# Performance work log

Hardware: AMD Instinct MI355X
Metric: run time of the kernel (lower is better)

## Reference

```python
import jax, jax.numpy as jnp
import numpy as np

N = 100000   # nodes
E = 1600000  # edges per view
F = 256      # feature_dim
G = 512      # num graphs in batch
H, C = 2, 32 # heads, channels per head (GATConv(F, 32, heads=2))
EPS = 1e-5


def setup_inputs() -> dict:
    key = jax.random.key(0)
    ks = jax.random.split(key, 32)
    def w(i, shape, fan_in):
        return jax.random.normal(ks[i], shape, jnp.float32) / np.sqrt(fan_in)
    inp = {
        "x": jax.random.normal(ks[0], (N, F), jnp.float32),
        "edge_index_ast": jax.random.randint(ks[1], (2, E), 0, N),
        "edge_index_cfg": jax.random.randint(ks[2], (2, E), 0, N),
        "edge_index_pdg": jax.random.randint(ks[3], (2, E), 0, N),
        "batch": jnp.sort(jax.random.randint(ks[4], (N,), 0, G)),
        "num_graphs": G,
        # BatchNorm1d(feature_dim) affine params (training-mode batch stats)
        "bn_w": jnp.ones((F,), jnp.float32),
        "bn_b": jnp.zeros((F,), jnp.float32),
    }
    i = 5
    for v in ("ast", "cfg", "pdg"):
        inp[f"{v}_W"] = w(i, (F, H * C), F); i += 1
        inp[f"{v}_att_src"] = w(i, (H, C), C); i += 1
        inp[f"{v}_att_dst"] = w(i, (H, C), C); i += 1
        inp[f"{v}_bias"] = jnp.zeros((H * C,), jnp.float32)
    inp["g1_w"] = w(i, (64, 32), 64); i += 1
    inp["g1_b"] = jnp.zeros((32,), jnp.float32)
    inp["g2_w"] = w(i, (32, 3), 32); i += 1
    inp["g2_b"] = jnp.zeros((3,), jnp.float32)
    inp["c1_w"] = w(i, (64, 128), 64); i += 1
    inp["c1_b"] = jnp.zeros((128,), jnp.float32)
    inp["c2_w"] = w(i, (128, 64), 128); i += 1
    inp["c2_b"] = jnp.zeros((64,), jnp.float32)
    inp["c3_w"] = w(i, (64, 1), 64); i += 1
    inp["c3_b"] = jnp.zeros((1,), jnp.float32)
    return inp


def _gat(x, edge_index, W, att_src, att_dst, bias):
    """PyG GATConv (shared lin, add_self_loops=True, concat heads)."""
    n = x.shape[0]
    loops = jnp.arange(n)
    src = jnp.concatenate([edge_index[0], loops])
    dst = jnp.concatenate([edge_index[1], loops])
    h = (x @ W).reshape(n, H, C)                       # [N,H,C]
    a_src = jnp.sum(h * att_src, axis=-1)              # [N,H]
    a_dst = jnp.sum(h * att_dst, axis=-1)              # [N,H]
    e = jax.nn.leaky_relu(a_src[src] + a_dst[dst], 0.2)  # [Etot,H]
    m = jax.ops.segment_max(e, dst, num_segments=n)
    p = jnp.exp(e - m[dst])
    denom = jax.ops.segment_sum(p, dst, num_segments=n)
    alpha = p / (denom[dst] + 1e-16)                   # [Etot,H]
    out = jax.ops.segment_sum(h[src] * alpha[:, :, None], dst, num_segments=n)
    return out.reshape(n, H * C) + bias


def reference(x, edge_index_ast, edge_index_cfg, edge_index_pdg, batch, num_graphs,
              bn_w, bn_b,
              ast_W, ast_att_src, ast_att_dst, ast_bias,
              cfg_W, cfg_att_src, cfg_att_dst, cfg_bias,
              pdg_W, pdg_att_src, pdg_att_dst, pdg_bias,
              g1_w, g1_b, g2_w, g2_b,
              c1_w, c1_b, c2_w, c2_b, c3_w, c3_b):
    # input BatchNorm1d (training-mode batch statistics, biased variance)
    mu = x.mean(0)
    var = x.var(0)
    xn = (x - mu) / jnp.sqrt(var + EPS) * bn_w + bn_b

    h_ast = jax.ops.segment_max(jax.nn.elu(_gat(xn, edge_index_ast, ast_W, ast_att_src, ast_att_dst, ast_bias)), batch, num_segments=num_graphs)
    h_cfg = jax.ops.segment_max(jax.nn.elu(_gat(xn, edge_index_cfg, cfg_W, cfg_att_src, cfg_att_dst, cfg_bias)), batch, num_segments=num_graphs)
    h_pdg = jax.ops.segment_max(jax.nn.elu(_gat(xn, edge_index_pdg, pdg_W, pdg_att_src, pdg_att_dst, pdg_bias)), batch, num_segments=num_graphs)

    avg_view = (h_ast + h_cfg + h_pdg) / 3.0
    wts = jax.nn.softmax(jax.nn.relu(avg_view @ g1_w + g1_b) @ g2_w + g2_b, axis=-1)
    fused = wts[:, 0:1] * h_ast + wts[:, 1:2] * h_cfg + wts[:, 2:3] * h_pdg

    # classifier (dropout = identity at inference)
    z = jax.nn.relu(fused @ c1_w + c1_b)
    z = jax.nn.relu(z @ c2_w + c2_b)
    logits = (z @ c3_w + c3_b).reshape(-1)             # [G]
    return logits
```

## Files before the change

### kernel.cpp

```cpp
#include <hip/hip_runtime.h>
#include <hip/hip_bf16.h>
#include <hip/hip_fp16.h>

#define N_NODES 100000
#define N_EDGES 1600000
#define ETOT    (N_EDGES + N_NODES)
#define NE3     (3 * ETOT)
#define N3      (3 * N_NODES)
#define NF      256
#define NG      512
#define NHC     64
#define NOUT3   192
#define BN_EPS  1e-5f

#define NBUCK   586
#define NB1     1024
#define EGRAIN  20
#define ECHUNK  (256 * EGRAIN)
#define SCAN_N  (NBUCK * NB1)
#define ATT_NB  (N3 * 16 / 256)

typedef _Float16 f16x8 __attribute__((ext_vector_type(8)));
typedef float    f32x4 __attribute__((ext_vector_type(4)));

__device__ __forceinline__ unsigned fenc(float f){
  unsigned b = __float_as_uint(f);
  return (b & 0x80000000u) ? ~b : (b | 0x80000000u);
}
__device__ __forceinline__ float fdec(unsigned u){
  unsigned b = (u & 0x80000000u) ? (u & 0x7FFFFFFFu) : ~u;
  return __uint_as_float(b);
}
__device__ __forceinline__ float lrelu(float x){ return x > 0.f ? x : 0.2f * x; }
__device__ __forceinline__ float eluf(float x){ return x > 0.f ? x : (__expf(x) - 1.f); }

__global__ void k_init_pooled(unsigned* pooled){
  int i = blockIdx.x * 256 + threadIdx.x;
  if (i < 3 * NG * NHC) pooled[i] = 0x007FFFFFu;
}

#define STATS_NB ((N_NODES + 127) / 128)
__global__ __launch_bounds__(256) void k_pre(const float* __restrict__ x,
                                             float* __restrict__ sums, float* __restrict__ sumsq,
                                             const int* __restrict__ eA, const int* __restrict__ eC,
                                             const int* __restrict__ eP,
                                             int* __restrict__ gcounts){
  int t = threadIdx.x;
  if (blockIdx.x < STATS_NB){
    int r0 = blockIdx.x * 128;
    int rmax = N_NODES - r0; if (rmax > 128) rmax = 128;
    float s = 0.f, q = 0.f;
    for (int r = 0; r < rmax; ++r){
      float v = x[(size_t)(r0 + r) * NF + t];
      s += v; q += v * v;
    }
    atomicAdd(&sums[t], s);
    atomicAdd(&sumsq[t], q);
    return;
  }
  __shared__ int hist[NBUCK];
  int bi = blockIdx.x - STATS_NB;
  for (int b = t; b < NBUCK; b += 256) hist[b] = 0;
  __syncthreads();
  int base = bi * ECHUNK + t;
#pragma unroll
  for (int k = 0; k < EGRAIN; ++k){
    int i = base + k * 256;
    if (i < NE3){
      int v = i / ETOT; int j = i - v * ETOT;
      const int* ei = (v == 0) ? eA : (v == 1) ? eC : eP;
      int d = (j < N_EDGES) ? ei[N_EDGES + j] : (j - N_EDGES);
      int vd = v * N_NODES + d;
      atomicAdd(&hist[vd >> 9], 1);
    }
  }
  __syncthreads();
  for (int b = t; b < NBUCK; b += 256) gcounts[b * NB1 + bi] = hist[b];
}

__global__ __launch_bounds__(256) void k_prep2(const float* __restrict__ sums, const float* __restrict__ sumsq,
                                               const float* __restrict__ bn_w, const float* __restrict__ bn_b,
                                               const float* __restrict__ WA, const float* __restrict__ WC,
                                               const float* __restrict__ WP,
                                               __half* __restrict__ WpT, float* __restrict__ bp){
  __shared__ float red[256];
  int o = blockIdx.x;
  int v = o >> 6, oc = o & 63;
  const float* W = (v == 0) ? WA : (v == 1) ? WC : WP;
  int f = threadIdx.x;
  float mu  = sums[f]  * (1.f / N_NODES);
  float var = sumsq[f] * (1.f / N_NODES) - mu * mu;
  float sc  = bn_w[f] * rsqrtf(var + BN_EPS);
  float sh_ = bn_b[f] - mu * sc;
  float w = W[f * 64 + oc];
  WpT[(size_t)o * NF + f] = __float2half(w * sc);
  red[f] = sh_ * w;
  __syncthreads();
  for (int off = 128; off > 0; off >>= 1){
    if (f < off) red[f] += red[f + off];
    __syncthreads();
  }
  if (f == 0) bp[o] = red[0];
}

__global__ __launch_bounds__(256) void k_scan1(const int* __restrict__ cnt, int* __restrict__ out,
                                               int* __restrict__ bsum, int n){
  __shared__ int sh[256];
  int t = threadIdx.x; int base = blockIdx.x * 2048 + t * 8;
  int v[8]; int s = 0;
#pragma unroll
  for (int i = 0; i < 8; ++i){ v[i] = (base + i < n) ? cnt[base + i] : 0; s += v[i]; }
  sh[t] = s; __syncthreads();
  for (int off = 1; off < 256; off <<= 1){
    int xv = (t >= off) ? sh[t - off] : 0;
    __syncthreads();
    sh[t] += xv;
    __syncthreads();
  }
  int p = sh[t] - s;
  if (t == 255) bsum[blockIdx.x] = sh[255];
#pragma unroll
  for (int i = 0; i < 8; ++i){ if (base + i < n) out[base + i] = p; p += v[i]; }
}

__global__ __launch_bounds__(512) void k_scan2(int* __restrict__ bsum, int* __restrict__ total_out, int nb){
  __shared__ int sh[512];
  int t = threadIdx.x;
  int o = (t < nb) ? bsum[t] : 0;
  sh[t] = o; __syncthreads();
  for (int off = 1; off < 512; off <<= 1){
    int xv = (t >= off) ? sh[t - off] : 0;
    __syncthreads();
    sh[t] += xv;
    __syncthreads();
  }
  if (t < nb) bsum[t] = sh[t] - o;
  if (t == nb - 1) total_out[0] = sh[t];
}

__global__ __launch_bounds__(256) void k_scan3(int* __restrict__ out, const int* __restrict__ bsum, int n){
  int add = bsum[blockIdx.x];
  int base = blockIdx.x * 2048 + threadIdx.x * 8;
#pragma unroll
  for (int i = 0; i < 8; ++i) if (base + i < n) out[base + i] += add;
}

#define GBM 64
#define GEMM_NB ((N_NODES + GBM - 1) / GBM)
__global__ __launch_bounds__(256) void k_fused(const float* __restrict__ x,
                                               const __half* __restrict__ WpT, const float* __restrict__ bp,
                                               __half* __restrict__ h16,
                                               const int* __restrict__ eA, const int* __restrict__ eC,
                                               const int* __restrict__ eP,
                                               const int* __restrict__ gscan, int* __restrict__ packed){
  union U { _Float16 xs[64 * 256]; int pos[NBUCK]; };
  __shared__ U sm;
  int t = threadIdx.x;
  if (blockIdx.x >= GEMM_NB){
    int bi = blockIdx.x - GEMM_NB;
    for (int b = t; b < NBUCK; b += 256) sm.pos[b] = gscan[b * NB1 + bi];
    __syncthreads();
    int base = bi * ECHUNK + t;
#pragma unroll
    for (int k = 0; k < EGRAIN; ++k){
      int i = base + k * 256;
      if (i < NE3){
        int v = i / ETOT; int j = i - v * ETOT;
        const int* ei = (v == 0) ? eA : (v == 1) ? eC : eP;
        int s, d;
        if (j < N_EDGES){ s = ei[j]; d = ei[N_EDGES + j]; } else { s = j - N_EDGES; d = s; }
        int vd = v * N_NODES + d;
        int p = atomicAdd(&sm.pos[vd >> 9], 1);
        packed[p] = s | ((vd & 511) << 17);
      }
    }
    return;
  }
  int m0 = blockIdx.x * GBM;
#pragma unroll
  for (int k = 0; k < 8; ++k){
    int G = t + k * 256;
    int row = G >> 5, g = G & 31;
    int grow = m0 + row; if (grow >= N_NODES) grow = N_NODES - 1;
    const float4* src = (const float4*)(x + (size_t)grow * NF + ((g ^ (row & 7)) << 3));
    float4 lo = src[0], hi = src[1];
    f16x8 h;
    h[0]=(_Float16)lo.x; h[1]=(_Float16)lo.y; h[2]=(_Float16)lo.z; h[3]=(_Float16)lo.w;
    h[4]=(_Float16)hi.x; h[5]=(_Float16)hi.y; h[6]=(_Float16)hi.z; h[7]=(_Float16)hi.w;
    *(f16x8*)&sm.xs[(size_t)G << 3] = h;
  }
  __syncthreads();
  int lane = t & 63, w = t >> 6;
  int lr = lane & 15, lk = lane >> 4;
  int colb = w * 48;
  f32x4 acc[4][3];
#pragma unroll
  for (int mt = 0; mt < 4; ++mt)
#pragma unroll
    for (int ct = 0; ct < 3; ++ct) acc[mt][ct] = (f32x4){0.f, 0.f, 0.f, 0.f};
  float bpv[3];
#pragma unroll
  for (int ct = 0; ct < 3; ++ct) bpv[ct] = bp[colb + ct * 16 + lr];
#pragma unroll
  for (int kk = 0; kk < 8; ++kk){
    int khalf = kk * 32 + lk * 8;
    f16x8 av[4];
#pragma unroll
    for (int mt = 0; mt < 4; ++mt){
      int row = mt * 16 + lr;
      av[mt] = *(const f16x8*)&sm.xs[row * 256 + (khalf ^ ((row & 7) << 3))];
    }
    f16x8 bv[3];
#pragma unroll
    for (int ct = 0; ct < 3; ++ct){
      int col = colb + ct * 16 + lr;
      bv[ct] = *(const f16x8*)(const void*)(WpT + (size_t)col * NF + khalf);
    }
#pragma unroll
    for (int mt = 0; mt < 4; ++mt)
#pragma unroll
      for (int ct = 0; ct < 3; ++ct)
        acc[mt][ct] = __builtin_amdgcn_mfma_f32_16x16x32_f16(av[mt], bv[ct], acc[mt][ct], 0, 0, 0);
  }
#pragma unroll
  for (int mt = 0; mt < 4; ++mt){
#pragma unroll
    for (int r = 0; r < 4; ++r){
      int row = m0 + mt * 16 + lk * 4 + r;
      if (row < N_NODES){
#pragma unroll
        for (int ct = 0; ct < 3; ++ct)
          h16[(size_t)row * NOUT3 + colb + ct * 16 + lr] = __float2half(acc[mt][ct][r] + bpv[ct]);
      }
    }
  }
}

__global__ __launch_bounds__(256) void k_build(const int* __restrict__ gscan, const int* __restrict__ packed,
                                               int* __restrict__ entries, int* __restrict__ offsets){
  __shared__ int hist2[512];
  __shared__ int sh[256];
  int b = blockIdx.x, t = threadIdx.x;
  int base = gscan[b * NB1];
  int end  = (b == NBUCK - 1) ? NE3 : gscan[(b + 1) * NB1];
  hist2[t * 2] = 0; hist2[t * 2 + 1] = 0;
  __syncthreads();
  for (int i = base + t; i < end; i += 256)
    atomicAdd(&hist2[(packed[i] >> 17) & 511], 1);
  __syncthreads();
  int s0 = hist2[t * 2], s1 = hist2[t * 2 + 1];
  int tot = s0 + s1;
  sh[t] = tot; __syncthreads();
  for (int off = 1; off < 256; off <<= 1){
    int xv = (t >= off) ? sh[t - off] : 0;
    __syncthreads();
    sh[t] += xv;
    __syncthreads();
  }
  int p = sh[t] - tot;
  hist2[t * 2]     = p;
  hist2[t * 2 + 1] = p + s0;
  __syncthreads();
#pragma unroll
  for (int i = 0; i < 2; ++i){
    int vd = (b << 9) + t * 2 + i;
    if (vd < N3) offsets[vd] = base + hist2[t * 2 + i];
  }
  if (b == NBUCK - 1 && t == 0) offsets[N3] = NE3;
  __syncthreads();
  for (int i = base + t; i < end; i += 256){
    int pk = packed[i];
    int low = (pk >> 17) & 511;
    int pos = atomicAdd(&hist2[low], 1);
    entries[base + pos] = pk & 0x1FFFF;
  }
}

__global__ __launch_bounds__(256) void k_att(const __half* __restrict__ h16,
                                             const float* __restrict__ asA, const float* __restrict__ adA,
                                             const float* __restrict__ asC, const float* __restrict__ adC,
                                             const float* __restrict__ asP, const float* __restrict__ adP,
                                             float* __restrict__ a_src, float* __restrict__ a_dst,
                                             unsigned* __restrict__ gpart){
  __shared__ unsigned samax[6];
  int t = threadIdx.x;
  if (t < 6) samax[t] = 0u;
  __syncthreads();
  int gt = blockIdx.x * 256 + t;
  int g = gt >> 4; int lid = gt & 15;
  int v = g / N_NODES; int n = g - v * N_NODES;
  const float* As = (v == 0) ? asA : (v == 1) ? asC : asP;
  const float* Ad = (v == 0) ? adA : (v == 1) ? adC : adP;
  const __half2* hp = (const __half2*)(h16 + (size_t)n * NOUT3 + v * 64 + lid * 4);
  float2 fa = __half22float2(hp[0]);
  float2 fb = __half22float2(hp[1]);
  float4 s4 = *(const float4*)(As + lid * 4);
  float4 d4 = *(const float4*)(Ad + lid * 4);
  float rs = fa.x*s4.x + fa.y*s4.y + fb.x*s4.z + fb.y*s4.w;
  float rd = fa.x*d4.x + fa.y*d4.y + fb.x*d4.z + fb.y*d4.w;
  rs += __shfl_xor(rs, 1); rd += __shfl_xor(rd, 1);
  rs += __shfl_xor(rs, 2); rd += __shfl_xor(rd, 2);
  rs += __shfl_xor(rs, 4); rd += __shfl_xor(rd, 4);
  if ((lid & 7) == 0){
    int h = lid >> 3;
    a_src[g * 2 + h] = rs;
    a_dst[g * 2 + h] = rd;
    atomicMax(&samax[v * 2 + h], fenc(rs));
  }
  __syncthreads();
  if (t < 6) gpart[blockIdx.x * 6 + t] = samax[t];
}

__global__ __launch_bounds__(256) void k_amax(const unsigned* __restrict__ gpart, unsigned* __restrict__ amax){
  __shared__ unsigned sm[6];
  int t = threadIdx.x;
  if (t < 6) sm[t] = 0u;
  __syncthreads();
  unsigned m[6] = {0u, 0u, 0u, 0u, 0u, 0u};
  for (int bi = t; bi < ATT_NB; bi += 256){
    const unsigned* p = gpart + (size_t)bi * 6;
#pragma unroll
    for (int k = 0; k < 6; ++k) m[k] = max(m[k], p[k]);
  }
#pragma unroll
  for (int k = 0; k < 6; ++k) atomicMax(&sm[k], m[k]);
  __syncthreads();
  if (t < 6) amax[t] = sm[t];
}

__global__ __launch_bounds__(256) void k_gather(const int* __restrict__ entries, const int* __restrict__ offsets,
                                                const float* __restrict__ a_src, const float* __restrict__ a_dst,
                                                const unsigned* __restrict__ amax,
                                                const __half* __restrict__ h16,
                                                const float* __restrict__ bA, const float* __restrict__ bC,
                                                const float* __restrict__ bP,
                                                const int* __restrict__ batch, unsigned* __restrict__ pooled){
  __shared__ unsigned red[64];
  __shared__ int kmin, kmax;
  int t = threadIdx.x;
  if (t == 0){ kmin = 0x7FFFFFFF; kmax = -1; }
  if (t < 64) red[t] = 0u;
  __syncthreads();
  int grp = t >> 4;
  int lid = t & 15;
  int g = blockIdx.x * 16 + grp;
  int v = g / N_NODES; int n = g - v * N_NODES;
  int vN = v * N_NODES;
  float ad0 = a_dst[g*2+0], ad1 = a_dst[g*2+1];
  float m0 = lrelu(fdec(amax[v*2+0]) + ad0);
  float m1 = lrelu(fdec(amax[v*2+1]) + ad1);
  int beg = offsets[g], end = offsets[g+1];
  int len = end - beg;
  float ax = 0.f, ay = 0.f, az = 0.f, aw = 0.f;
  float den0 = 0.f, den1 = 0.f;
  const __half* hbase = h16 + v * 64 + lid * 4;
  for (int c0 = 0; c0 < len; c0 += 16){
    int nc = len - c0; if (nc > 16) nc = 16;
    int s_ = 0; float p0 = 0.f, p1 = 0.f;
    if (lid < nc){
      s_ = entries[beg + c0 + lid];
      float2 ap = *(const float2*)(a_src + (size_t)(vN + s_) * 2);
      p0 = __expf(lrelu(ap.x + ad0) - m0);
      p1 = __expf(lrelu(ap.y + ad1) - m1);
    }
    den0 += p0; den1 += p1;
    for (int k = 0; k < nc; k += 4){
      uint2 r[4]; float pav[4], pbv[4];
#pragma unroll
      for (int j = 0; j < 4; ++j){
        int kk = k + j;
        int sk = __shfl(s_, kk, 16);
        r[j] = *(const uint2*)(hbase + (size_t)sk * NOUT3);
        pav[j] = __shfl(p0, kk, 16);
        pbv[j] = __shfl(p1, kk, 16);
      }
#pragma unroll
      for (int j = 0; j < 4; ++j){
        int kk = k + j;
        if (kk < nc){
          float ph = (lid < 8) ? pav[j] : pbv[j];
          float2 fa2 = __half22float2(*(__half2*)&r[j].x);
          float2 fb2 = __half22float2(*(__half2*)&r[j].y);
          ax += ph * fa2.x; ay += ph * fa2.y; az += ph * fb2.x; aw += ph * fb2.y;
        }
      }
    }
  }
#pragma unroll
  for (int msk = 1; msk < 16; msk <<= 1){
    den0 += __shfl_xor(den0, msk);
    den1 += __shfl_xor(den1, msk);
  }
  float den = ((lid < 8) ? den0 : den1) + 1e-16f;
  const float* bias = (v == 0) ? bA : (v == 1) ? bC : bP;
  float4 b4 = *(const float4*)(bias + lid * 4);
  unsigned e0u = fenc(eluf(ax / den + b4.x));
  unsigned e1u = fenc(eluf(ay / den + b4.y));
  unsigned e2u = fenc(eluf(az / den + b4.z));
  unsigned e3u = fenc(eluf(aw / den + b4.w));
  int key = v * NG + batch[n];
  if (lid == 0){ atomicMin(&kmin, key); atomicMax(&kmax, key); }
  atomicMax(&red[lid*4+0], e0u); atomicMax(&red[lid*4+1], e1u);
  atomicMax(&red[lid*4+2], e2u); atomicMax(&red[lid*4+3], e3u);
  __syncthreads();
  if (kmin == kmax){
    if (t < 64) atomicMax(&pooled[(size_t)kmin * 64 + t], red[t]);
  } else {
    unsigned* pp = pooled + (size_t)key * 64 + lid * 4;
    atomicMax(pp+0, e0u); atomicMax(pp+1, e1u); atomicMax(pp+2, e2u); atomicMax(pp+3, e3u);
  }
}

__global__ __launch_bounds__(64) void k_head(const unsigned* __restrict__ pooled,
                                             const float* __restrict__ g1w, const float* __restrict__ g1b,
                                             const float* __restrict__ g2w, const float* __restrict__ g2b,
                                             const float* __restrict__ c1w, const float* __restrict__ c1b,
                                             const float* __restrict__ c2w, const float* __restrict__ c2b,
                                             const float* __restrict__ c3w, const float* __restrict__ c3b,
                                             float* __restrict__ out){
  __shared__ float s1[64];
  __shared__ float s2[128];
  __shared__ float sw[3];
  int g = blockIdx.x, l = threadIdx.x;
  float ha = fdec(pooled[(size_t)g * 64 + l]);
  float hc = fdec(pooled[(size_t)(NG + g) * 64 + l]);
  float hp = fdec(pooled[(size_t)(2 * NG + g) * 64 + l]);
  s1[l] = (ha + hc + hp) * (1.f / 3.f);
  __syncthreads();
  float r1 = 0.f;
  if (l < 32){
    r1 = g1b[l];
    for (int i = 0; i < 64; ++i) r1 += s1[i] * g1w[i * 32 + l];
    r1 = fmaxf(r1, 0.f);
  }
  __syncthreads();
  if (l < 32) s2[l] = r1;
  __syncthreads();
  if (l < 3){
    float tv = g2b[l];
    for (int i = 0; i < 32; ++i) tv += s2[i] * g2w[i * 3 + l];
    sw[l] = tv;
  }
  __syncthreads();
  float t0 = sw[0], t1 = sw[1], t2 = sw[2];
  float mx = fmaxf(t0, fmaxf(t1, t2));
  float w0 = __expf(t0 - mx), w1 = __expf(t1 - mx), w2 = __expf(t2 - mx);
  float wsum = w0 + w1 + w2;
  float fused = (w0 * ha + w1 * hc + w2 * hp) / wsum;
  __syncthreads();
  s1[l] = fused;
  __syncthreads();
  float za = c1b[l], zb = c1b[64 + l];
  for (int i = 0; i < 64; ++i){
    float f = s1[i];
    za += f * c1w[i * 128 + l];
    zb += f * c1w[i * 128 + 64 + l];
  }
  za = fmaxf(za, 0.f); zb = fmaxf(zb, 0.f);
  s2[l] = za; s2[64 + l] = zb;
  __syncthreads();
  float z2 = c2b[l];
  for (int i = 0; i < 128; ++i) z2 += s2[i] * c2w[i * 64 + l];
  z2 = fmaxf(z2, 0.f);
  float prod = z2 * c3w[l];
  for (int off = 32; off > 0; off >>= 1) prod += __shfl_down(prod, off);
  if (l == 0) out[g] = prod + c3b[0];
}

extern "C" void kernel_launch(void* const* d_in, const int* in_sizes, int n_in,
                              void* d_out, int out_size, void* d_ws, size_t ws_size,
                              hipStream_t stream){
  const float* x    = (const float*)d_in[0];
  const int* eA     = (const int*)d_in[1];
  const int* eC     = (const int*)d_in[2];
  const int* eP     = (const int*)d_in[3];
  const int* batch  = (const int*)d_in[4];
  const float* bn_w = (const float*)d_in[6];
  const float* bn_b = (const float*)d_in[7];
  const float* WA   = (const float*)d_in[8];
  const float* asA  = (const float*)d_in[9];
  const float* adA  = (const float*)d_in[10];
  const float* bA   = (const float*)d_in[11];
  const float* WC   = (const float*)d_in[12];
  const float* asC  = (const float*)d_in[13];
  const float* adC  = (const float*)d_in[14];
  const float* bC   = (const float*)d_in[15];
  const float* WP   = (const float*)d_in[16];
  const float* asP  = (const float*)d_in[17];
  const float* adP  = (const float*)d_in[18];
  const float* bP   = (const float*)d_in[19];
  const float* g1w  = (const float*)d_in[20];
  const float* g1b  = (const float*)d_in[21];
  const float* g2w  = (const float*)d_in[22];
  const float* g2b  = (const float*)d_in[23];
  const float* c1w  = (const float*)d_in[24];
  const float* c1b  = (const float*)d_in[25];
  const float* c2w  = (const float*)d_in[26];
  const float* c2b  = (const float*)d_in[27];
  const float* c3w  = (const float*)d_in[28];
  const float* c3b  = (const float*)d_in[29];
  float* out = (float*)d_out;

  char* wptr = (char*)d_ws;
  auto alloc = [&](size_t bytes) -> void* {
    void* p = (void*)wptr;
    wptr += (bytes + 255) & ~(size_t)255;
    return p;
  };
  float*    sums    = (float*)   alloc((size_t)NF * 4);
  float*    sumsq   = (float*)   alloc((size_t)NF * 4);
  size_t zbytes = (size_t)(wptr - (char*)sums);
  int*      gcounts = (int*)     alloc((size_t)SCAN_N * 4);
  int*      gscan   = (int*)     alloc((size_t)SCAN_N * 4);
  int*      offsets = (int*)     alloc(((size_t)N3 + 1) * 4);
  __half*   WpT     = (__half*)  alloc((size_t)NOUT3 * NF * 2);
  float*    bp      = (float*)   alloc((size_t)NOUT3 * 4);
  __half*   h16     = (__half*)  alloc((size_t)N_NODES * NOUT3 * 2);
  float*    a_src   = (float*)   alloc((size_t)N3 * 2 * 4);
  float*    a_dst   = (float*)   alloc((size_t)N3 * 2 * 4);
  int*      packed  = (int*)     alloc((size_t)NE3 * 4);
  int*      entries = (int*)     alloc((size_t)NE3 * 4);
  unsigned* pooled  = (unsigned*)alloc((size_t)3 * NG * NHC * 4);
  unsigned* gpart   = (unsigned*)alloc((size_t)ATT_NB * 6 * 4);
  unsigned* amax    = (unsigned*)alloc((size_t)64 * 4);
  int*      bsum    = (int*)     alloc((size_t)512 * 4);
  int*      scrtot  = (int*)     alloc((size_t)64 * 4);

  hipMemsetAsync(sums, 0, zbytes, stream);
  k_init_pooled<<<(3 * NG * NHC + 255) / 256, 256, 0, stream>>>(pooled);
  k_pre<<<STATS_NB + NB1, 256, 0, stream>>>(x, sums, sumsq, eA, eC, eP, gcounts);
  k_prep2<<<NOUT3, 256, 0, stream>>>(sums, sumsq, bn_w, bn_b, WA, WC, WP, WpT, bp);
  int nb_sc = (SCAN_N + 2047) / 2048;
  k_scan1<<<nb_sc, 256, 0, stream>>>(gcounts, gscan, bsum, SCAN_N);
  k_scan2<<<1, 512, 0, stream>>>(bsum, scrtot, nb_sc);
  k_scan3<<<nb_sc, 256, 0, stream>>>(gscan, bsum, SCAN_N);
  k_fused<<<GEMM_NB + NB1, 256, 0, stream>>>(x, WpT, bp, h16, eA, eC, eP, gscan, packed);
  k_att<<<ATT_NB, 256, 0, stream>>>(h16, asA, adA, asC, adC, asP, adP, a_src, a_dst, gpart);
  k_amax<<<1, 256, 0, stream>>>(gpart, amax);
  k_build<<<NBUCK, 256, 0, stream>>>(gscan, packed, entries, offsets);
  k_gather<<<N3 / 16, 256, 0, stream>>>(entries, offsets, a_src, a_dst, amax, h16, bA, bC, bP, batch, pooled);
  k_head<<<NG, 64, 0, stream>>>(pooled, g1w, g1b, g2w, g2b, c1w, c1b, c2w, c2b, c3w, c3b, out);
}
```

Before: 377.5 us.

## Widen CSR buckets, fuse amax into build, deterministic BN stats, unroll gather

Several independent changes ship together. Buckets now cover 1024 destination nodes each, halving the bucket count, and k_build runs 512 threads per block; the separate single-block k_amax reduction is folded into block 0 of k_build. BatchNorm column sums are written as per-block partials and reduced by a new k_stats2 kernel, which replaces global atomics and the memset. The gather inner loop is unrolled by 8 using precomputed byte offsets and FMAs, and drops the per-element bound check: out-of-range lanes carry zero weight and load row 0, so some loads are wasted.

```diff
diff --git a/kernel.cpp b/kernel.cpp
--- a/kernel.cpp
+++ b/kernel.cpp
@@ -13,7 +13,7 @@
 #define NOUT3   192
 #define BN_EPS  1e-5f
 
-#define NBUCK   586
+#define NBUCK   293
 #define NB1     1024
 #define EGRAIN  20
 #define ECHUNK  (256 * EGRAIN)
@@ -41,7 +41,7 @@
 
 #define STATS_NB ((N_NODES + 127) / 128)
 __global__ __launch_bounds__(256) void k_pre(const float* __restrict__ x,
-                                             float* __restrict__ sums, float* __restrict__ sumsq,
+                                             float* __restrict__ spartS, float* __restrict__ spartQ,
                                              const int* __restrict__ eA, const int* __restrict__ eC,
                                              const int* __restrict__ eP,
                                              int* __restrict__ gcounts){
@@ -54,8 +54,8 @@
       float v = x[(size_t)(r0 + r) * NF + t];
       s += v; q += v * v;
     }
-    atomicAdd(&sums[t], s);
-    atomicAdd(&sumsq[t], q);
+    spartS[(size_t)t * STATS_NB + blockIdx.x] = s;
+    spartQ[(size_t)t * STATS_NB + blockIdx.x] = q;
     return;
   }
   __shared__ int hist[NBUCK];
@@ -71,11 +71,29 @@
       const int* ei = (v == 0) ? eA : (v == 1) ? eC : eP;
       int d = (j < N_EDGES) ? ei[N_EDGES + j] : (j - N_EDGES);
       int vd = v * N_NODES + d;
-      atomicAdd(&hist[vd >> 9], 1);
+      atomicAdd(&hist[vd >> 10], 1);
     }
   }
   __syncthreads();
   for (int b = t; b < NBUCK; b += 256) gcounts[b * NB1 + bi] = hist[b];
+}
+
+__global__ __launch_bounds__(256) void k_stats2(const float* __restrict__ spartS, const float* __restrict__ spartQ,
+                                                float* __restrict__ sums, float* __restrict__ sumsq){
+  __shared__ float rs[256], rq[256];
+  int c = blockIdx.x, i = threadIdx.x;
+  float s = 0.f, q = 0.f;
+  for (int b = i; b < STATS_NB; b += 256){
+    s += spartS[(size_t)c * STATS_NB + b];
+    q += spartQ[(size_t)c * STATS_NB + b];
+  }
+  rs[i] = s; rq[i] = q;
+  __syncthreads();
+  for (int off = 128; off > 0; off >>= 1){
+    if (i < off){ rs[i] += rs[i + off]; rq[i] += rq[i + off]; }
+    __syncthreads();
+  }
+  if (i == 0){ sums[c] = rs[0]; sumsq[c] = rq[0]; }
 }
 
 __global__ __launch_bounds__(256) void k_prep2(const float* __restrict__ sums, const float* __restrict__ sumsq,
@@ -170,8 +188,8 @@
         int s, d;
         if (j < N_EDGES){ s = ei[j]; d = ei[N_EDGES + j]; } else { s = j - N_EDGES; d = s; }
         int vd = v * N_NODES + d;
-        int p = atomicAdd(&sm.pos[vd >> 9], 1);
-        packed[p] = s | ((vd & 511) << 17);
+        int p = atomicAdd(&sm.pos[vd >> 10], 1);
+        packed[p] = s | ((vd & 1023) << 17);
       }
     }
     return;
@@ -233,46 +251,6 @@
           h16[(size_t)row * NOUT3 + colb + ct * 16 + lr] = __float2half(acc[mt][ct][r] + bpv[ct]);
       }
     }
-  }
-}
-
-__global__ __launch_bounds__(256) void k_build(const int* __restrict__ gscan, const int* __restrict__ packed,
-                                               int* __restrict__ entries, int* __restrict__ offsets){
-  __shared__ int hist2[512];
-  __shared__ int sh[256];
-  int b = blockIdx.x, t = threadIdx.x;
-  int base = gscan[b * NB1];
-  int end  = (b == NBUCK - 1) ? NE3 : gscan[(b + 1) * NB1];
-  hist2[t * 2] = 0; hist2[t * 2 + 1] = 0;
-  __syncthreads();
-  for (int i = base + t; i < end; i += 256)
-    atomicAdd(&hist2[(packed[i] >> 17) & 511], 1);
-  __syncthreads();
-  int s0 = hist2[t * 2], s1 = hist2[t * 2 + 1];
-  int tot = s0 + s1;
-  sh[t] = tot; __syncthreads();
-  for (int off = 1; off < 256; off <<= 1){
-    int xv = (t >= off) ? sh[t - off] : 0;
-    __syncthreads();
-    sh[t] += xv;
-    __syncthreads();
-  }
-  int p = sh[t] - tot;
-  hist2[t * 2]     = p;
-  hist2[t * 2 + 1] = p + s0;
-  __syncthreads();
-#pragma unroll
-  for (int i = 0; i < 2; ++i){
-    int vd = (b << 9) + t * 2 + i;
-    if (vd < N3) offsets[vd] = base + hist2[t * 2 + i];
-  }
-  if (b == NBUCK - 1 && t == 0) offsets[N3] = NE3;
-  __syncthreads();
-  for (int i = base + t; i < end; i += 256){
-    int pk = packed[i];
-    int low = (pk >> 17) & 511;
-    int pos = atomicAdd(&hist2[low], 1);
-    entries[base + pos] = pk & 0x1FFFF;
   }
 }
 
@@ -311,21 +289,57 @@
   if (t < 6) gpart[blockIdx.x * 6 + t] = samax[t];
 }
 
-__global__ __launch_bounds__(256) void k_amax(const unsigned* __restrict__ gpart, unsigned* __restrict__ amax){
-  __shared__ unsigned sm[6];
-  int t = threadIdx.x;
-  if (t < 6) sm[t] = 0u;
-  __syncthreads();
-  unsigned m[6] = {0u, 0u, 0u, 0u, 0u, 0u};
-  for (int bi = t; bi < ATT_NB; bi += 256){
-    const unsigned* p = gpart + (size_t)bi * 6;
-#pragma unroll
-    for (int k = 0; k < 6; ++k) m[k] = max(m[k], p[k]);
-  }
-#pragma unroll
-  for (int k = 0; k < 6; ++k) atomicMax(&sm[k], m[k]);
-  __syncthreads();
-  if (t < 6) amax[t] = sm[t];
+__global__ __launch_bounds__(512) void k_build(const int* __restrict__ gscan, const int* __restrict__ packed,
+                                               int* __restrict__ entries, int* __restrict__ offsets,
+                                               const unsigned* __restrict__ gpart, unsigned* __restrict__ amax){
+  __shared__ int hist2[1024];
+  __shared__ int sh[512];
+  __shared__ unsigned smx[6];
+  int b = blockIdx.x, t = threadIdx.x;
+  if (b == 0){
+    if (t < 6) smx[t] = 0u;
+    __syncthreads();
+    unsigned m[6] = {0u, 0u, 0u, 0u, 0u, 0u};
+    for (int bi = t; bi < ATT_NB; bi += 512){
+      const unsigned* p = gpart + (size_t)bi * 6;
+#pragma unroll
+      for (int k = 0; k < 6; ++k) m[k] = max(m[k], p[k]);
+    }
+#pragma unroll
+    for (int k = 0; k < 6; ++k) atomicMax(&smx[k], m[k]);
+    __syncthreads();
+    if (t < 6) amax[t] = smx[t];
+  }
+  int base = gscan[b * NB1];
+  int end  = (b == NBUCK - 1) ? NE3 : gscan[(b + 1) * NB1];
+  hist2[t * 2] = 0; hist2[t * 2 + 1] = 0;
+  __syncthreads();
+  for (int i = base + t; i < end; i += 512)
+    atomicAdd(&hist2[(packed[i] >> 17) & 1023], 1);
+  __syncthreads();
+  int s0 = hist2[t * 2], s1 = hist2[t * 2 + 1];
+  int tot = s0 + s1;
+  sh[t] = tot; __syncthreads();
+  for (int off = 1; off < 512; off <<= 1){
+    int xv = (t >= off) ? sh[t - off] : 0;
+    __syncthreads();
+    sh[t] += xv;
+    __syncthreads();
+  }
+  int excl = sh[t] - tot;
+  hist2[t * 2]     = excl;
+  hist2[t * 2 + 1] = excl + s0;
+  int vd0 = (b << 10) + t * 2;
+  if (vd0 < N3)     offsets[vd0]     = base + excl;
+  if (vd0 + 1 < N3) offsets[vd0 + 1] = base + excl + s0;
+  if (b == NBUCK - 1 && t == 0) offsets[N3] = NE3;
+  __syncthreads();
+  for (int i = base + t; i < end; i += 512){
+    int pk = packed[i];
+    int low = (pk >> 17) & 1023;
+    int pos = atomicAdd(&hist2[low], 1);
+    entries[base + pos] = pk & 0x1FFFF;
+  }
 }
 
 __global__ __launch_bounds__(256) void k_gather(const int* __restrict__ entries, const int* __restrict__ offsets,
@@ -353,36 +367,37 @@
   int len = end - beg;
   float ax = 0.f, ay = 0.f, az = 0.f, aw = 0.f;
   float den0 = 0.f, den1 = 0.f;
-  const __half* hbase = h16 + v * 64 + lid * 4;
+  const char* hb = (const char*)h16;
+  unsigned lconst = (unsigned)((v << 7) + (lid << 3));
   for (int c0 = 0; c0 < len; c0 += 16){
     int nc = len - c0; if (nc > 16) nc = 16;
-    int s_ = 0; float p0 = 0.f, p1 = 0.f;
+    unsigned off_ = 0u;
+    float p0f = 0.f, p1f = 0.f;
     if (lid < nc){
-      s_ = entries[beg + c0 + lid];
+      int s_ = entries[beg + c0 + lid];
       float2 ap = *(const float2*)(a_src + (size_t)(vN + s_) * 2);
-      p0 = __expf(lrelu(ap.x + ad0) - m0);
-      p1 = __expf(lrelu(ap.y + ad1) - m1);
-    }
-    den0 += p0; den1 += p1;
-    for (int k = 0; k < nc; k += 4){
-      uint2 r[4]; float pav[4], pbv[4];
-#pragma unroll
-      for (int j = 0; j < 4; ++j){
+      p0f = __expf(lrelu(ap.x + ad0) - m0);
+      p1f = __expf(lrelu(ap.y + ad1) - m1);
+      off_ = (unsigned)s_ * (NOUT3 * 2);
+    }
+    den0 += p0f; den1 += p1f;
+    for (int k = 0; k < nc; k += 8){
+      uint2 r[8]; float pa[8];
+#pragma unroll
+      for (int j = 0; j < 8; ++j){
         int kk = k + j;
-        int sk = __shfl(s_, kk, 16);
-        r[j] = *(const uint2*)(hbase + (size_t)sk * NOUT3);
-        pav[j] = __shfl(p0, kk, 16);
-        pbv[j] = __shfl(p1, kk, 16);
+        unsigned ob = (unsigned)__shfl((int)off_, kk, 16) + lconst;
+        float pA = __shfl(p0f, kk, 16);
+        float pB = __shfl(p1f, kk, 16);
+        r[j] = *(const uint2*)(hb + ob);
+        pa[j] = (lid < 8) ? pA : pB;
       }
 #pragma unroll
-      for (int j = 0; j < 4; ++j){
-        int kk = k + j;
-        if (kk < nc){
-          float ph = (lid < 8) ? pav[j] : pbv[j];
-          float2 fa2 = __half22float2(*(__half2*)&r[j].x);
-          float2 fb2 = __half22float2(*(__half2*)&r[j].y);
-          ax += ph * fa2.x; ay += ph * fa2.y; az += ph * fb2.x; aw += ph * fb2.y;
-        }
+      for (int j = 0; j < 8; ++j){
+        float2 fa2 = __half22float2(*(__half2*)&r[j].x);
+        float2 fb2 = __half22float2(*(__half2*)&r[j].y);
+        ax = fmaf(pa[j], fa2.x, ax); ay = fmaf(pa[j], fa2.y, ay);
+        az = fmaf(pa[j], fb2.x, az); aw = fmaf(pa[j], fb2.y, aw);
       }
     }
   }
@@ -509,7 +524,8 @@
   };
   float*    sums    = (float*)   alloc((size_t)NF * 4);
   float*    sumsq   = (float*)   alloc((size_t)NF * 4);
-  size_t zbytes = (size_t)(wptr - (char*)sums);
+  float*    spartS  = (float*)   alloc((size_t)NF * STATS_NB * 4);
+  float*    spartQ  = (float*)   alloc((size_t)NF * STATS_NB * 4);
   int*      gcounts = (int*)     alloc((size_t)SCAN_N * 4);
   int*      gscan   = (int*)     alloc((size_t)SCAN_N * 4);
   int*      offsets = (int*)     alloc(((size_t)N3 + 1) * 4);
@@ -526,9 +542,9 @@
   int*      bsum    = (int*)     alloc((size_t)512 * 4);
   int*      scrtot  = (int*)     alloc((size_t)64 * 4);
 
-  hipMemsetAsync(sums, 0, zbytes, stream);
   k_init_pooled<<<(3 * NG * NHC + 255) / 256, 256, 0, stream>>>(pooled);
-  k_pre<<<STATS_NB + NB1, 256, 0, stream>>>(x, sums, sumsq, eA, eC, eP, gcounts);
+  k_pre<<<STATS_NB + NB1, 256, 0, stream>>>(x, spartS, spartQ, eA, eC, eP, gcounts);
+  k_stats2<<<NF, 256, 0, stream>>>(spartS, spartQ, sums, sumsq);
   k_prep2<<<NOUT3, 256, 0, stream>>>(sums, sumsq, bn_w, bn_b, WA, WC, WP, WpT, bp);
   int nb_sc = (SCAN_N + 2047) / 2048;
   k_scan1<<<nb_sc, 256, 0, stream>>>(gcounts, gscan, bsum, SCAN_N);
@@ -536,8 +552,7 @@
   k_scan3<<<nb_sc, 256, 0, stream>>>(gscan, bsum, SCAN_N);
   k_fused<<<GEMM_NB + NB1, 256, 0, stream>>>(x, WpT, bp, h16, eA, eC, eP, gscan, packed);
   k_att<<<ATT_NB, 256, 0, stream>>>(h16, asA, adA, asC, adC, asP, adP, a_src, a_dst, gpart);
-  k_amax<<<1, 256, 0, stream>>>(gpart, amax);
-  k_build<<<NBUCK, 256, 0, stream>>>(gscan, packed, entries, offsets);
+  k_build<<<NBUCK, 512, 0, stream>>>(gscan, packed, entries, offsets, gpart, amax);
   k_gather<<<N3 / 16, 256, 0, stream>>>(entries, offsets, a_src, a_dst, amax, h16, bA, bC, bP, batch, pooled);
   k_head<<<NG, 64, 0, stream>>>(pooled, g1w, g1b, g2w, g2b, c1w, c1b, c2w, c2b, c3w, c3b, out);
 }
```

After: 330.2 us. 1.14x faster.
